# Kernel tuning notes

Hardware: AMD Instinct MI355X
Metric: run time of the kernel (lower is better)

## Reference

```python
import jax, jax.numpy as jnp
import numpy as np

B, N, D = 2, 50000, 16
E = N * D  # total flattened neighbor entries


def setup_inputs() -> dict:
    key = jax.random.key(0)
    k1, k2, k3, k4 = jax.random.split(key, 4)
    xyz1 = jax.random.normal(k1, (B, N, 3), dtype=jnp.float32)
    # deformed coordinates = rest + small displacement (realistic ARAP setting)
    xyz2 = xyz1 + 0.1 * jax.random.normal(k2, (B, N, 3), dtype=jnp.float32)
    neighborList = jax.random.randint(k3, (E,), 0, N, dtype=jnp.int32)
    numNeighbors = jnp.full((N,), D, dtype=jnp.int32)
    accnumNeighbors = jnp.concatenate(
        [jnp.zeros((1,), jnp.int32), jnp.cumsum(numNeighbors)[:-1].astype(jnp.int32)])
    weightMatrix = jax.random.uniform(k4, (E,), dtype=jnp.float32)
    eye9 = jnp.eye(3, dtype=jnp.float32).reshape(9)
    rotations = jnp.broadcast_to(eye9, (B, N, 9))
    return {
        "xyz1": xyz1, "xyz2": xyz2, "neighborList": neighborList,
        "numNeighbors": numNeighbors, "accnumNeighbors": accnumNeighbors,
        "weightMatrix": weightMatrix, "rotations": rotations, "arapWeight": 1,
    }


def _arap_rotations(xyz1, xyz2, neighborList, numNeighbors, weightMatrix):
    b, n, _ = xyz1.shape
    e = neighborList.shape[0]
    # CSR segment ids: vertex id owning each flattened neighbor entry
    seg = jnp.repeat(jnp.arange(n, dtype=jnp.int32), numNeighbors, total_repeat_length=e)
    d1 = xyz1[:, seg] - xyz1[:, neighborList]   # [B,E,3] rest-pose edge vectors
    d2 = xyz2[:, seg] - xyz2[:, neighborList]   # [B,E,3] deformed edge vectors
    # weighted covariance contributions S_e = w_e * d1 d2^T : [B,E,3,3]
    outer = weightMatrix[None, :, None, None] * d1[..., :, None] * d2[..., None, :]
    # per-vertex covariance S_i = sum_{j in N(i)} S_e : [B,N,3,3]
    S = jax.vmap(lambda o: jax.ops.segment_sum(o, seg, num_segments=n))(outer)
    # Procrustes fit: R = V U^T with reflection fix
    U, s, Vt = jnp.linalg.svd(S)
    V = jnp.swapaxes(Vt, -1, -2)
    Ut = jnp.swapaxes(U, -1, -2)
    R = V @ Ut
    det = jnp.linalg.det(R)                      # [B,N]
    V = V.at[..., :, 2].multiply(jnp.where(det < 0, -1.0, 1.0)[..., None])
    R = V @ Ut
    return R.reshape(b, n, 9)


def reference(xyz1, xyz2, neighborList, numNeighbors, accnumNeighbors,
              weightMatrix, rotations, arapWeight):
    # accnumNeighbors (prefix offsets), rotations (initial guess) and arapWeight
    # are consumed by the CUDA kernel for addressing / loss weighting but do not
    # change the fitted rotations; the math is the ARAP local step below.
    return _arap_rotations(xyz1, xyz2, neighborList, numNeighbors, weightMatrix)
```

## Files before the change

### kernel.cpp

```cpp
#include <hip/hip_runtime.h>
#include <hip/hip_bf16.h>


__global__ __launch_bounds__(256)
void prepack_kernel(const float* __restrict__ xyz1,
                    const float* __restrict__ xyz2,
                    float4* __restrict__ pk,
                    int total)
{
    int t = blockIdx.x * blockDim.x + threadIdx.x;
    if (t >= total) return;
    float4 a, c;
    a.x = xyz1[t * 3 + 0]; a.y = xyz1[t * 3 + 1]; a.z = xyz1[t * 3 + 2]; a.w = 0.f;
    c.x = xyz2[t * 3 + 0]; c.y = xyz2[t * 3 + 1]; c.z = xyz2[t * 3 + 2]; c.w = 0.f;
    pk[2 * (size_t)t + 0] = a;
    pk[2 * (size_t)t + 1] = c;
}

__global__ __launch_bounds__(256)
void gather_kernel(const float4* __restrict__ pk,
                   const int*   __restrict__ nbr,
                   const int*   __restrict__ num,
                   const int*   __restrict__ acc,
                   const float* __restrict__ wgt,
                   float*       __restrict__ Sout,
                   int B, int N)
{
    int tid = blockIdx.x * blockDim.x + threadIdx.x;
    int v = tid >> 4;
    int k = tid & 15;
    int total = B * N;
    if (v >= total) return;
    int b = v / N;
    int i = v - b * N;

    const float4* base = pk + 2 * (size_t)b * N;
    float4 P1 = base[2 * i + 0];
    float4 P2 = base[2 * i + 1];

    int a0  = acc[i];
    int cnt = num[i];

    float Sxx = 0.f, Sxy = 0.f, Sxz = 0.f;
    float Syx = 0.f, Syy = 0.f, Syz = 0.f;
    float Szx = 0.f, Szy = 0.f, Szz = 0.f;

    for (int kk = k; kk < cnt; kk += 16) {
        int   e  = a0 + kk;
        int   j  = nbr[e];
        float we = wgt[e];
        float4 A = base[2 * j + 0];
        float4 C = base[2 * j + 1];
        float d1x = P1.x - A.x, d1y = P1.y - A.y, d1z = P1.z - A.z;
        float d2x = P2.x - C.x, d2y = P2.y - C.y, d2z = P2.z - C.z;
        float w1x = we * d1x, w1y = we * d1y, w1z = we * d1z;
        Sxx += w1x * d2x;  Sxy += w1x * d2y;  Sxz += w1x * d2z;
        Syx += w1y * d2x;  Syy += w1y * d2y;  Syz += w1y * d2z;
        Szx += w1z * d2x;  Szy += w1z * d2y;  Szz += w1z * d2z;
    }

#pragma unroll
    for (int m = 8; m >= 1; m >>= 1) {
        Sxx += __shfl_xor(Sxx, m);  Sxy += __shfl_xor(Sxy, m);  Sxz += __shfl_xor(Sxz, m);
        Syx += __shfl_xor(Syx, m);  Syy += __shfl_xor(Syy, m);  Syz += __shfl_xor(Syz, m);
        Szx += __shfl_xor(Szx, m);  Szy += __shfl_xor(Szy, m);  Szz += __shfl_xor(Szz, m);
    }

    if (k == 0) {
        size_t st = (size_t)total;
        Sout[0 * st + v] = Sxx;  Sout[1 * st + v] = Sxy;  Sout[2 * st + v] = Sxz;
        Sout[3 * st + v] = Syx;  Sout[4 * st + v] = Syy;  Sout[5 * st + v] = Syz;
        Sout[6 * st + v] = Szx;  Sout[7 * st + v] = Szy;  Sout[8 * st + v] = Szz;
    }
}

__global__ __launch_bounds__(256)
void solve_kernel(const float* __restrict__ Sin,
                  float*       __restrict__ out,
                  int total)
{
    int t = blockIdx.x * blockDim.x + threadIdx.x;
    if (t >= total) return;
    size_t st = (size_t)total;
    float Sxx = Sin[0 * st + t], Sxy = Sin[1 * st + t], Sxz = Sin[2 * st + t];
    float Syx = Sin[3 * st + t], Syy = Sin[4 * st + t], Syz = Sin[5 * st + t];
    float Szx = Sin[6 * st + t], Szy = Sin[7 * st + t], Szz = Sin[8 * st + t];

    float n00 =  Sxx + Syy + Szz;
    float n01 =  Syz - Szy;
    float n02 =  Szx - Sxz;
    float n03 =  Sxy - Syx;
    float n11 =  Sxx - Syy - Szz;
    float n12 =  Sxy + Syx;
    float n13 =  Szx + Sxz;
    float n22 = -Sxx + Syy - Szz;
    float n23 =  Syz + Szy;
    float n33 = -Sxx - Syy + Szz;

    float fro2 = Sxx*Sxx + Sxy*Sxy + Sxz*Sxz
               + Syx*Syx + Syy*Syy + Syz*Syz
               + Szx*Szx + Szy*Szy + Szz*Szz;
    float s = 2.0f * sqrtf(fro2) + 1e-30f;

    float m00 = n00 + s, m01 = n01, m02 = n02, m03 = n03;
    float m11 = n11 + s, m12 = n12, m13 = n13;
    float m22 = n22 + s, m23 = n23;
    float m33 = n33 + s;

    {
        float inv = 1.0f / (m00 + m11 + m22 + m33);
        m00 *= inv; m01 *= inv; m02 *= inv; m03 *= inv;
        m11 *= inv; m12 *= inv; m13 *= inv;
        m22 *= inv; m23 *= inv; m33 *= inv;
    }

#pragma unroll
    for (int it = 0; it < 16; ++it) {
        float p00 = m00*m00 + m01*m01 + m02*m02 + m03*m03;
        float p01 = m00*m01 + m01*m11 + m02*m12 + m03*m13;
        float p02 = m00*m02 + m01*m12 + m02*m22 + m03*m23;
        float p03 = m00*m03 + m01*m13 + m02*m23 + m03*m33;
        float p11 = m01*m01 + m11*m11 + m12*m12 + m13*m13;
        float p12 = m01*m02 + m11*m12 + m12*m22 + m13*m23;
        float p13 = m01*m03 + m11*m13 + m12*m23 + m13*m33;
        float p22 = m02*m02 + m12*m12 + m22*m22 + m23*m23;
        float p23 = m02*m03 + m12*m13 + m22*m23 + m23*m33;
        float p33 = m03*m03 + m13*m13 + m23*m23 + m33*m33;
        float inv = 1.0f / (p00 + p11 + p22 + p33);
        m00 = p00 * inv; m01 = p01 * inv; m02 = p02 * inv; m03 = p03 * inv;
        m11 = p11 * inv; m12 = p12 * inv; m13 = p13 * inv;
        m22 = p22 * inv; m23 = p23 * inv;
        m33 = p33 * inv;
    }

    float qw = m00, qx = m01, qy = m02, qz = m03, best = m00;
    {
        bool g = m11 > best;
        qw = g ? m01 : qw; qx = g ? m11 : qx; qy = g ? m12 : qy; qz = g ? m13 : qz;
        best = g ? m11 : best;
        g = m22 > best;
        qw = g ? m02 : qw; qx = g ? m12 : qx; qy = g ? m22 : qy; qz = g ? m23 : qz;
        best = g ? m22 : best;
        g = m33 > best;
        qw = g ? m03 : qw; qx = g ? m13 : qx; qy = g ? m23 : qy; qz = g ? m33 : qz;
    }
    {
        float inv = rsqrtf(qw*qw + qx*qx + qy*qy + qz*qz);
        qw *= inv; qx *= inv; qy *= inv; qz *= inv;
    }

    float xx = qx*qx, yy = qy*qy, zz = qz*qz;
    float xy = qx*qy, xz = qx*qz, yz = qy*qz;
    float wx = qw*qx, wy = qw*qy, wz = qw*qz;

    float* o = out + (size_t)t * 9;
    o[0] = 1.f - 2.f*(yy + zz);
    o[1] = 2.f*(xy - wz);
    o[2] = 2.f*(xz + wy);
    o[3] = 2.f*(xy + wz);
    o[4] = 1.f - 2.f*(xx + zz);
    o[5] = 2.f*(yz - wx);
    o[6] = 2.f*(xz - wy);
    o[7] = 2.f*(yz + wx);
    o[8] = 1.f - 2.f*(xx + yy);
}

extern "C" void kernel_launch(void* const* d_in, const int* in_sizes, int n_in,
                              void* d_out, int out_size, void* d_ws, size_t ws_size,
                              hipStream_t stream) {
    const float* xyz1 = (const float*)d_in[0];
    const float* xyz2 = (const float*)d_in[1];
    const int*   nbr  = (const int*)  d_in[2];
    const int*   num  = (const int*)  d_in[3];
    const int*   acc  = (const int*)  d_in[4];
    const float* wgt  = (const float*)d_in[5];
    float* out = (float*)d_out;

    int N = in_sizes[3];
    int B = in_sizes[0] / (N * 3);
    int total = B * N;

    float4* pk = (float4*)d_ws;
    float*  Sb = (float*)((char*)d_ws + (size_t)total * 32);

    int block = 256;
    prepack_kernel<<<(total + block - 1) / block, block, 0, stream>>>(
        xyz1, xyz2, pk, total);
    int gthreads = total * 16;
    gather_kernel<<<(gthreads + block - 1) / block, block, 0, stream>>>(
        pk, nbr, num, acc, wgt, Sb, B, N);
    solve_kernel<<<(total + block - 1) / block, block, 0, stream>>>(
        Sb, out, total);
}
```

Measured before the change: 100.6 us.

## Fuse neighbor gather and rotation solve into one kernel with 4 threads per vertex

Merges the covariance gather and the quaternion eigen-solve into a single kernel, removing the intermediate S buffer round trip and one launch. Each vertex is now handled by 4 lanes instead of 16, each loading its 4 neighbor indices and weights with a single vectorized int4/float4 load when the count is 16 and the offset is aligned. The redundant solve runs on all 4 lanes and only lane 0 writes. The trade-off is fewer threads in flight for hiding the random gather latency and 4x duplicated solve arithmetic.

```diff
diff --git a/kernel.cpp b/kernel.cpp
--- a/kernel.cpp
+++ b/kernel.cpp
@@ -18,17 +18,17 @@
 }
 
 __global__ __launch_bounds__(256)
-void gather_kernel(const float4* __restrict__ pk,
-                   const int*   __restrict__ nbr,
-                   const int*   __restrict__ num,
-                   const int*   __restrict__ acc,
-                   const float* __restrict__ wgt,
-                   float*       __restrict__ Sout,
-                   int B, int N)
+void arap_fused_kernel(const float4* __restrict__ pk,
+                       const int*   __restrict__ nbr,
+                       const int*   __restrict__ num,
+                       const int*   __restrict__ acc,
+                       const float* __restrict__ wgt,
+                       float*       __restrict__ out,
+                       int B, int N)
 {
     int tid = blockIdx.x * blockDim.x + threadIdx.x;
-    int v = tid >> 4;
-    int k = tid & 15;
+    int v = tid >> 2;
+    int u = tid & 3;
     int total = B * N;
     if (v >= total) return;
     int b = v / N;
@@ -45,46 +45,46 @@
     float Syx = 0.f, Syy = 0.f, Syz = 0.f;
     float Szx = 0.f, Szy = 0.f, Szz = 0.f;
 
-    for (int kk = k; kk < cnt; kk += 16) {
-        int   e  = a0 + kk;
-        int   j  = nbr[e];
-        float we = wgt[e];
-        float4 A = base[2 * j + 0];
-        float4 C = base[2 * j + 1];
-        float d1x = P1.x - A.x, d1y = P1.y - A.y, d1z = P1.z - A.z;
-        float d2x = P2.x - C.x, d2y = P2.y - C.y, d2z = P2.z - C.z;
-        float w1x = we * d1x, w1y = we * d1y, w1z = we * d1z;
-        Sxx += w1x * d2x;  Sxy += w1x * d2y;  Sxz += w1x * d2z;
-        Syx += w1y * d2x;  Syy += w1y * d2y;  Syz += w1y * d2z;
-        Szx += w1z * d2x;  Szy += w1z * d2y;  Szz += w1z * d2z;
+    if (cnt == 16 && (a0 & 3) == 0) {
+        int4   jj = ((const int4*)(nbr + a0))[u];
+        float4 ww = ((const float4*)(wgt + a0))[u];
+        int   js[4] = {jj.x, jj.y, jj.z, jj.w};
+        float ws[4] = {ww.x, ww.y, ww.z, ww.w};
+#pragma unroll
+        for (int r = 0; r < 4; ++r) {
+            int j = js[r];
+            float4 A = base[2 * j + 0];
+            float4 C = base[2 * j + 1];
+            float we = ws[r];
+            float d1x = P1.x - A.x, d1y = P1.y - A.y, d1z = P1.z - A.z;
+            float d2x = P2.x - C.x, d2y = P2.y - C.y, d2z = P2.z - C.z;
+            float w1x = we * d1x, w1y = we * d1y, w1z = we * d1z;
+            Sxx += w1x * d2x;  Sxy += w1x * d2y;  Sxz += w1x * d2z;
+            Syx += w1y * d2x;  Syy += w1y * d2y;  Syz += w1y * d2z;
+            Szx += w1z * d2x;  Szy += w1z * d2y;  Szz += w1z * d2z;
+        }
+    } else {
+        for (int kk = u; kk < cnt; kk += 4) {
+            int   e  = a0 + kk;
+            int   j  = nbr[e];
+            float we = wgt[e];
+            float4 A = base[2 * j + 0];
+            float4 C = base[2 * j + 1];
+            float d1x = P1.x - A.x, d1y = P1.y - A.y, d1z = P1.z - A.z;
+            float d2x = P2.x - C.x, d2y = P2.y - C.y, d2z = P2.z - C.z;
+            float w1x = we * d1x, w1y = we * d1y, w1z = we * d1z;
+            Sxx += w1x * d2x;  Sxy += w1x * d2y;  Sxz += w1x * d2z;
+            Syx += w1y * d2x;  Syy += w1y * d2y;  Syz += w1y * d2z;
+            Szx += w1z * d2x;  Szy += w1z * d2y;  Szz += w1z * d2z;
+        }
     }
 
 #pragma unroll
-    for (int m = 8; m >= 1; m >>= 1) {
+    for (int m = 2; m >= 1; m >>= 1) {
         Sxx += __shfl_xor(Sxx, m);  Sxy += __shfl_xor(Sxy, m);  Sxz += __shfl_xor(Sxz, m);
         Syx += __shfl_xor(Syx, m);  Syy += __shfl_xor(Syy, m);  Syz += __shfl_xor(Syz, m);
         Szx += __shfl_xor(Szx, m);  Szy += __shfl_xor(Szy, m);  Szz += __shfl_xor(Szz, m);
     }
-
-    if (k == 0) {
-        size_t st = (size_t)total;
-        Sout[0 * st + v] = Sxx;  Sout[1 * st + v] = Sxy;  Sout[2 * st + v] = Sxz;
-        Sout[3 * st + v] = Syx;  Sout[4 * st + v] = Syy;  Sout[5 * st + v] = Syz;
-        Sout[6 * st + v] = Szx;  Sout[7 * st + v] = Szy;  Sout[8 * st + v] = Szz;
-    }
-}
-
-__global__ __launch_bounds__(256)
-void solve_kernel(const float* __restrict__ Sin,
-                  float*       __restrict__ out,
-                  int total)
-{
-    int t = blockIdx.x * blockDim.x + threadIdx.x;
-    if (t >= total) return;
-    size_t st = (size_t)total;
-    float Sxx = Sin[0 * st + t], Sxy = Sin[1 * st + t], Sxz = Sin[2 * st + t];
-    float Syx = Sin[3 * st + t], Syy = Sin[4 * st + t], Syz = Sin[5 * st + t];
-    float Szx = Sin[6 * st + t], Szy = Sin[7 * st + t], Szz = Sin[8 * st + t];
 
     float n00 =  Sxx + Syy + Szz;
     float n01 =  Syz - Szy;
@@ -149,20 +149,21 @@
         qw *= inv; qx *= inv; qy *= inv; qz *= inv;
     }
 
-    float xx = qx*qx, yy = qy*qy, zz = qz*qz;
-    float xy = qx*qy, xz = qx*qz, yz = qy*qz;
-    float wx = qw*qx, wy = qw*qy, wz = qw*qz;
-
-    float* o = out + (size_t)t * 9;
-    o[0] = 1.f - 2.f*(yy + zz);
-    o[1] = 2.f*(xy - wz);
-    o[2] = 2.f*(xz + wy);
-    o[3] = 2.f*(xy + wz);
-    o[4] = 1.f - 2.f*(xx + zz);
-    o[5] = 2.f*(yz - wx);
-    o[6] = 2.f*(xz - wy);
-    o[7] = 2.f*(yz + wx);
-    o[8] = 1.f - 2.f*(xx + yy);
+    if (u == 0) {
+        float xx = qx*qx, yy = qy*qy, zz = qz*qz;
+        float xy = qx*qy, xz = qx*qz, yz = qy*qz;
+        float wx = qw*qx, wy = qw*qy, wz = qw*qz;
+        float* o = out + (size_t)v * 9;
+        o[0] = 1.f - 2.f*(yy + zz);
+        o[1] = 2.f*(xy - wz);
+        o[2] = 2.f*(xz + wy);
+        o[3] = 2.f*(xy + wz);
+        o[4] = 1.f - 2.f*(xx + zz);
+        o[5] = 2.f*(yz - wx);
+        o[6] = 2.f*(xz - wy);
+        o[7] = 2.f*(yz + wx);
+        o[8] = 1.f - 2.f*(xx + yy);
+    }
 }
 
 extern "C" void kernel_launch(void* const* d_in, const int* in_sizes, int n_in,
@@ -181,14 +182,11 @@
     int total = B * N;
 
     float4* pk = (float4*)d_ws;
-    float*  Sb = (float*)((char*)d_ws + (size_t)total * 32);
 
     int block = 256;
     prepack_kernel<<<(total + block - 1) / block, block, 0, stream>>>(
         xyz1, xyz2, pk, total);
-    int gthreads = total * 16;
-    gather_kernel<<<(gthreads + block - 1) / block, block, 0, stream>>>(
-        pk, nbr, num, acc, wgt, Sb, B, N);
-    solve_kernel<<<(total + block - 1) / block, block, 0, stream>>>(
-        Sb, out, total);
+    int fthreads = total * 4;
+    arap_fused_kernel<<<(fthreads + block - 1) / block, block, 0, stream>>>(
+        pk, nbr, num, acc, wgt, out, B, N);
 }
```

Measured after the change: 101.7 us. No clear change (+1.1%).
